# Kernel tuning notes

Measured on AMD Instinct MI355X. Metric: run time of the kernel, lower is better.

## Reference

```python
import jax, jax.numpy as jnp
import numpy as np

N = 4096          # nodes (= Mamba sequence length)
E_EDGES = 65536   # edges
D = 512           # dim_h (= d_inner, expand=1)
NEXP = 4          # num_experts (cfg.model.num_experts)
DSTATE = 16
DCONV = 4
DTRANK = 32       # ceil(D/16)
EPS = 1e-5


def _silu(x):
    return x * jax.nn.sigmoid(x)


def _bn(h, g, b):
    # BatchNorm1d over node axis (batch statistics)
    mu = h.mean(0)
    var = h.var(0)
    return (h - mu) * jax.lax.rsqrt(var + EPS) * g + b


def _mamba(u, in_w, conv_w, conv_b, x_w, dt_w, dt_b, A_log, Dp, out_w):
    # u: [L, D] single-sequence Mamba(d_model=D, d_state=16, d_conv=4, expand=1)
    L = u.shape[0]
    xz = u @ in_w                      # [L, 2D]
    xc, z = xz[:, :D], xz[:, D:]
    xp = jnp.pad(xc, ((DCONV - 1, 0), (0, 0)))
    xconv = conv_b
    for k in range(DCONV):             # depthwise causal conv, tiny fixed loop
        xconv = xconv + conv_w[:, k] * xp[k:k + L]
    xs = _silu(xconv)                  # [L, D]
    dbc = xs @ x_w                     # [L, DTRANK + 2*DSTATE]
    dt = jax.nn.softplus(dbc[:, :DTRANK] @ dt_w + dt_b)          # [L, D]
    Bm = dbc[:, DTRANK:DTRANK + DSTATE]                          # [L, S]
    Cm = dbc[:, DTRANK + DSTATE:]                                # [L, S]
    A = -jnp.exp(A_log)                                          # [D, S]
    dA = jnp.exp(dt[:, :, None] * A[None])                       # [L, D, S]
    dBu = dt[:, :, None] * Bm[:, None, :] * xs[:, :, None]       # [L, D, S]

    def step(hprev, inp):
        dA_t, dBu_t, C_t = inp
        hn = dA_t * hprev + dBu_t
        return hn, (hn * C_t[None, :]).sum(-1)

    _, ys = jax.lax.scan(step, jnp.zeros((D, DSTATE), u.dtype), (dA, dBu, Cm))
    y = ys + Dp * xs
    return (y * _silu(z)) @ out_w      # [L, D]


def setup_inputs() -> dict:
    key = jax.random.key(0)
    ks = jax.random.split(key, 24)
    s = 1.0 / np.sqrt(D)
    inp = {}
    inp['x'] = jax.random.normal(ks[0], (N, D), jnp.float32)
    inp['edge_index'] = jax.random.randint(ks[1], (2, E_EDGES), 0, N)
    inp['edge_attr'] = jax.random.normal(ks[2], (E_EDGES, D), jnp.float32)
    # GINE nn: Linear(D,D) -> ReLU -> Linear(D,D)
    inp['gin_w1'] = jax.random.normal(ks[3], (D, D)) * s
    inp['gin_b1'] = jnp.zeros((D,))
    inp['gin_w2'] = jax.random.normal(ks[4], (D, D)) * s
    inp['gin_b2'] = jnp.zeros((D,))
    # BatchNorms
    inp['bn1l_g'] = jnp.ones((D,)); inp['bn1l_b'] = jnp.zeros((D,))
    inp['bn1a_g'] = jnp.ones((D,)); inp['bn1a_b'] = jnp.zeros((D,))
    inp['bn2_g'] = jnp.ones((D,)); inp['bn2_b'] = jnp.zeros((D,))
    # gating MLP [D, D//2, NEXP]
    inp['gate_w1'] = jax.random.normal(ks[5], (D, D // 2)) * s
    inp['gate_b1'] = jnp.zeros((D // 2,))
    inp['gate_w2'] = jax.random.normal(ks[6], (D // 2, NEXP)) * (1.0 / np.sqrt(D // 2))
    inp['gate_b2'] = jnp.zeros((NEXP,))
    # stacked per-expert Mamba params
    inp['in_w'] = jax.random.normal(ks[7], (NEXP, D, 2 * D)) * s
    inp['conv_w'] = jax.random.normal(ks[8], (NEXP, D, DCONV)) * 0.5
    inp['conv_b'] = jnp.zeros((NEXP, D))
    inp['x_w'] = jax.random.normal(ks[9], (NEXP, D, DTRANK + 2 * DSTATE)) * s
    inp['dt_w'] = jax.random.normal(ks[10], (NEXP, DTRANK, D)) * (1.0 / np.sqrt(DTRANK))
    inp['dt_b'] = jax.random.normal(ks[11], (NEXP, D)) * 0.1 - 4.0
    A0 = jnp.log(jnp.arange(1, DSTATE + 1, dtype=jnp.float32))
    inp['A_log'] = jnp.broadcast_to(A0, (NEXP, D, DSTATE)).copy()
    inp['Dp'] = jnp.ones((NEXP, D))
    inp['out_w'] = jax.random.normal(ks[12], (NEXP, D, D)) * s
    # FFN
    inp['ff_w1'] = jax.random.normal(ks[13], (D, 2 * D)) * s
    inp['ff_b1'] = jnp.zeros((2 * D,))
    inp['ff_w2'] = jax.random.normal(ks[14], (2 * D, D)) * (1.0 / np.sqrt(2 * D))
    inp['ff_b2'] = jnp.zeros((D,))
    return inp


def reference(x, edge_index, edge_attr,
              gin_w1, gin_b1, gin_w2, gin_b2,
              bn1l_g, bn1l_b, bn1a_g, bn1a_b, bn2_g, bn2_b,
              gate_w1, gate_b1, gate_w2, gate_b2,
              in_w, conv_w, conv_b, x_w, dt_w, dt_b, A_log, Dp, out_w,
              ff_w1, ff_b1, ff_w2, ff_b2):
    h_in = x
    src, dst = edge_index[0], edge_index[1]
    # local GINEConv: nn(x + sum_j relu(x_j + e_ji))
    msg = jax.nn.relu(x[src] + edge_attr)                      # [E, D]
    aggr = jax.ops.segment_sum(msg, dst, num_segments=N)       # [N, D]
    h_local = jax.nn.relu((x + aggr) @ gin_w1 + gin_b1) @ gin_w2 + gin_b2
    h_local = _bn(h_in + h_local, bn1l_g, bn1l_b)
    # gated mixture of Mamba experts
    gate = jax.nn.softmax(jax.nn.relu(x @ gate_w1 + gate_b1) @ gate_w2 + gate_b2, axis=-1)  # [N, NEXP]
    ys = jax.vmap(_mamba, in_axes=(None, 0, 0, 0, 0, 0, 0, 0, 0, 0))(
        x, in_w, conv_w, conv_b, x_w, dt_w, dt_b, A_log, Dp, out_w)  # [NEXP, N, D]
    h_attn = jnp.einsum('ne,end->nd', gate, ys)
    h_attn = _bn(h_in + h_attn, bn1a_g, bn1a_b)
    # fuse + FFN
    h = h_local + h_attn
    ff = jax.nn.relu(h @ ff_w1 + ff_b1) @ ff_w2 + ff_b2
    return _bn(h + ff, bn2_g, bn2_b)
```

## Files before the change

### kernel.cpp

```cpp
#include <hip/hip_runtime.h>
#include <hip/hip_bf16.h>
#include <math.h>

#define N_NODES 4096
#define E_EDGE 65536
#define D 512
#define NEXP 4
#define DSTATE 16
#define DCONV 4
#define DTRANK 32
#define EPS 1e-5f
#define LCHUNK 32
#define NCHUNK (N_NODES / LCHUNK)

typedef __hip_bfloat16 bf16;
typedef short bf16x8 __attribute__((ext_vector_type(8)));
typedef float f32x4 __attribute__((ext_vector_type(4)));
typedef unsigned short u16x4 __attribute__((ext_vector_type(4)));

__device__ __forceinline__ float siluf(float x) { return x / (1.f + __expf(-x)); }
__device__ __forceinline__ float softplusf(float x) {
  return (x > 20.f) ? x : log1pf(__expf(x));
}
__device__ __forceinline__ unsigned short f2bf(float v) {
  bf16 b = __float2bfloat16(v);
  return *reinterpret_cast<unsigned short*>(&b);
}
__device__ __forceinline__ float bfu2f(unsigned short u) {
  bf16 b;
  *reinterpret_cast<unsigned short*>(&b) = u;
  return __bfloat162float(b);
}

__device__ __forceinline__ void gload16(const void* g, void* l) {
  __builtin_amdgcn_global_load_lds(
      (const __attribute__((address_space(1))) void*)g,
      (__attribute__((address_space(3))) void*)l, 16, 0, 0);
}

template <int FN, int EPI, bool STATS>
__global__ __launch_bounds__(256, 2) void mm_k(
    const bf16* __restrict__ A, int lda, long sA,
    const bf16* __restrict__ Bt, int ldb, long sB,
    const float* __restrict__ bias,
    float* __restrict__ Cf, bf16* __restrict__ Cb, int ldc, long sC, int K,
    const float* __restrict__ part, float* __restrict__ sacc) {
  constexpr int BN = FN * 32;
  __shared__ __align__(16) bf16 As[2][128 * 32];
  __shared__ __align__(16) bf16 Bs[2][BN * 32];
  const int z = blockIdx.z;
  A += (size_t)z * sA;
  Bt += (size_t)z * sB;
  const int tid = threadIdx.x;
  const int w = tid >> 6, l = tid & 63;
  const int wr = w >> 1, wc = w & 1;
  const int bm = blockIdx.y * 128, bn = blockIdx.x * BN;

  f32x4 acc[4][FN];
#pragma unroll
  for (int i = 0; i < 4; ++i)
#pragma unroll
    for (int j = 0; j < FN; ++j) acc[i][j] = 0.f;

  const int srow = l >> 2, schunk = l & 3;
  const bf16* gA = A + (size_t)(bm + w * 16 + srow) * lda + schunk * 8;
  const bf16* gB = Bt + (size_t)(bn + w * 16 + srow) * ldb + schunk * 8;

  const int ar = wr * 64 + (l & 15);
  const int br = wc * FN * 16 + (l & 15);
  const int kb = l >> 4;

  auto stage = [&](int b, int k0) {
    gload16(gA + k0, As[b] + w * 512);
    gload16(gA + k0 + (size_t)64 * lda, As[b] + 64 * 32 + w * 512);
    gload16(gB + k0, Bs[b] + w * 512);
    if (FN == 4) gload16(gB + k0 + (size_t)64 * ldb, Bs[b] + 64 * 32 + w * 512);
  };

  stage(0, 0);
  __syncthreads();
  int cur = 0;
  for (int k0 = 0; k0 < K; k0 += 32) {
    if (k0 + 32 < K) stage(cur ^ 1, k0 + 32);
    const bf16x8* Ap = (const bf16x8*)As[cur];
    const bf16x8* Bp = (const bf16x8*)Bs[cur];
    bf16x8 af[4], bfr[FN];
#pragma unroll
    for (int i = 0; i < 4; ++i) af[i] = Ap[(ar + i * 16) * 4 + kb];
#pragma unroll
    for (int j = 0; j < FN; ++j) bfr[j] = Bp[(br + j * 16) * 4 + kb];
#pragma unroll
    for (int i = 0; i < 4; ++i)
#pragma unroll
      for (int j = 0; j < FN; ++j)
        acc[i][j] = __builtin_amdgcn_mfma_f32_16x16x32_bf16(bfr[j], af[i], acc[i][j], 0, 0, 0);
    __syncthreads();
    cur ^= 1;
  }

  if (Cf) Cf += (size_t)z * sC;
  if (Cb) Cb += (size_t)z * sC;
  const int r0 = bm + wr * 64 + (l & 15);
  const int cb0 = bn + wc * FN * 16 + ((l >> 4) << 2);
  f32x4 ssum[FN], ssq[FN];
  if (STATS) {
#pragma unroll
    for (int j = 0; j < FN; ++j) { ssum[j] = 0.f; ssq[j] = 0.f; }
  }
#pragma unroll
  for (int i = 0; i < 4; ++i) {
    const int row = r0 + i * 16;
#pragma unroll
    for (int j = 0; j < FN; ++j) {
      const int col = cb0 + j * 16;
      f32x4 v = acc[i][j];
      if (bias) v += *(const f32x4*)&bias[col];
      if (EPI == 1) {
#pragma unroll
        for (int r = 0; r < 4; ++r) v[r] = fmaxf(v[r], 0.f);
      }
      if (Cf) *(f32x4*)&Cf[(size_t)row * ldc + col] = v;
      if (Cb) {
        u16x4 u;
#pragma unroll
        for (int r = 0; r < 4; ++r) u[r] = f2bf(v[r]);
        *(u16x4*)&Cb[(size_t)row * ldc + col] = u;
      }
      if (STATS) {
        f32x4 p = *(const f32x4*)&part[(size_t)row * ldc + col];
        f32x4 t = v + p;
        ssum[j] += t;
        ssq[j] += t * t;
      }
    }
  }
  if (STATS) {
#pragma unroll
    for (int m = 1; m < 16; m <<= 1) {
#pragma unroll
      for (int j = 0; j < FN; ++j)
#pragma unroll
        for (int r = 0; r < 4; ++r) {
          ssum[j][r] += __shfl_xor(ssum[j][r], m);
          ssq[j][r] += __shfl_xor(ssq[j][r], m);
        }
    }
    if ((l & 15) == 0) {
#pragma unroll
      for (int j = 0; j < FN; ++j)
#pragma unroll
        for (int r = 0; r < 4; ++r) {
          atomicAdd(&sacc[cb0 + j * 16 + r], ssum[j][r]);
          atomicAdd(&sacc[512 + cb0 + j * 16 + r], ssq[j][r]);
        }
    }
  }
}

struct MmArgs {
  const bf16* A[4];
  const bf16* Bt[4];
  const float* bias[4];
  float* Cf[4];
  bf16* Cb[4];
  const float* part[4];
  float* sacc[4];
  long sA[4], sB[4], sC[4];
  int lda[4], ldb[4], ldc[4], K[4], epi[4], stats[4], gx[4], cum[4];
};
__global__ __launch_bounds__(256, 2) void mgemm_k(MmArgs a) {
  __shared__ __align__(16) bf16 As[2][128 * 32];
  __shared__ __align__(16) bf16 Bs[2][64 * 32];
  int b = blockIdx.x;
  int i = 0;
  while (b >= a.cum[i]) ++i;
  int local = b - (i ? a.cum[i - 1] : 0);
  const int perz = a.gx[i] * 32;
  const int z = local / perz;
  const int rem = local - z * perz;
  const int by = rem / a.gx[i];
  const int bx = rem - by * a.gx[i];
  const int lda = a.lda[i], ldb = a.ldb[i], ldc = a.ldc[i], K = a.K[i];
  const bf16* A = a.A[i] + (size_t)z * a.sA[i];
  const bf16* Bt = a.Bt[i] + (size_t)z * a.sB[i];

  const int tid = threadIdx.x;
  const int w = tid >> 6, l = tid & 63;
  const int wr = w >> 1, wc = w & 1;
  const int bm = by * 128, bn = bx * 64;

  f32x4 acc[4][2];
#pragma unroll
  for (int p = 0; p < 4; ++p)
#pragma unroll
    for (int j = 0; j < 2; ++j) acc[p][j] = 0.f;

  const int srow = l >> 2, schunk = l & 3;
  const bf16* gA = A + (size_t)(bm + w * 16 + srow) * lda + schunk * 8;
  const bf16* gB = Bt + (size_t)(bn + w * 16 + srow) * ldb + schunk * 8;

  const int ar = wr * 64 + (l & 15);
  const int br = wc * 32 + (l & 15);
  const int kb = l >> 4;

  auto stage = [&](int bb, int k0) {
    gload16(gA + k0, As[bb] + w * 512);
    gload16(gA + k0 + (size_t)64 * lda, As[bb] + 64 * 32 + w * 512);
    gload16(gB + k0, Bs[bb] + w * 512);
  };

  stage(0, 0);
  __syncthreads();
  int cur = 0;
  for (int k0 = 0; k0 < K; k0 += 32) {
    if (k0 + 32 < K) stage(cur ^ 1, k0 + 32);
    const bf16x8* Ap = (const bf16x8*)As[cur];
    const bf16x8* Bp = (const bf16x8*)Bs[cur];
    bf16x8 af[4], bfr[2];
#pragma unroll
    for (int p = 0; p < 4; ++p) af[p] = Ap[(ar + p * 16) * 4 + kb];
#pragma unroll
    for (int j = 0; j < 2; ++j) bfr[j] = Bp[(br + j * 16) * 4 + kb];
#pragma unroll
    for (int p = 0; p < 4; ++p)
#pragma unroll
      for (int j = 0; j < 2; ++j)
        acc[p][j] = __builtin_amdgcn_mfma_f32_16x16x32_bf16(bfr[j], af[p], acc[p][j], 0, 0, 0);
    __syncthreads();
    cur ^= 1;
  }

  float* Cf = a.Cf[i] ? a.Cf[i] + (size_t)z * a.sC[i] : nullptr;
  bf16* Cb = a.Cb[i] ? a.Cb[i] + (size_t)z * a.sC[i] : nullptr;
  const float* bias = a.bias[i];
  const int epi = a.epi[i], stats = a.stats[i];
  const int r0 = bm + wr * 64 + (l & 15);
  const int cb0 = bn + wc * 32 + ((l >> 4) << 2);
  f32x4 ssum[2], ssq[2];
  ssum[0] = 0.f; ssum[1] = 0.f; ssq[0] = 0.f; ssq[1] = 0.f;
#pragma unroll
  for (int p = 0; p < 4; ++p) {
    const int row = r0 + p * 16;
#pragma unroll
    for (int j = 0; j < 2; ++j) {
      const int col = cb0 + j * 16;
      f32x4 v = acc[p][j];
      if (bias) v += *(const f32x4*)&bias[col];
      if (epi == 1) {
#pragma unroll
        for (int r = 0; r < 4; ++r) v[r] = fmaxf(v[r], 0.f);
      }
      if (Cf) *(f32x4*)&Cf[(size_t)row * ldc + col] = v;
      if (Cb) {
        u16x4 u;
#pragma unroll
        for (int r = 0; r < 4; ++r) u[r] = f2bf(v[r]);
        *(u16x4*)&Cb[(size_t)row * ldc + col] = u;
      }
      if (stats) {
        f32x4 pp = *(const f32x4*)&a.part[i][(size_t)row * ldc + col];
        f32x4 t = v + pp;
        ssum[j] += t;
        ssq[j] += t * t;
      }
    }
  }
  if (stats) {
#pragma unroll
    for (int m = 1; m < 16; m <<= 1) {
#pragma unroll
      for (int j = 0; j < 2; ++j)
#pragma unroll
        for (int r = 0; r < 4; ++r) {
          ssum[j][r] += __shfl_xor(ssum[j][r], m);
          ssq[j][r] += __shfl_xor(ssq[j][r], m);
        }
    }
    if ((l & 15) == 0) {
#pragma unroll
      for (int j = 0; j < 2; ++j)
#pragma unroll
        for (int r = 0; r < 4; ++r) {
          atomicAdd(&a.sacc[i][cb0 + j * 16 + r], ssum[j][r]);
          atomicAdd(&a.sacc[i][512 + cb0 + j * 16 + r], ssq[j][r]);
        }
    }
  }
}

struct WtArgs {
  const float* in[8];
  bf16* out[8];
  int K[8], N[8], ldo[8];
  long sin[8], sout[8];
  int cum[8];
};
__global__ __launch_bounds__(256) void wtrans_all_k(WtArgs a) {
  __shared__ float t[32][33];
  int b = blockIdx.x;
  int i = 0;
  while (b >= a.cum[i]) ++i;
  int local = b - (i ? a.cum[i - 1] : 0);
  const int ntx = a.N[i] / 32;
  const int nty = a.K[i] / 32;
  const int perz = ntx * nty;
  const int z = local / perz;
  const int rem = local - z * perz;
  const int bx = rem % ntx, by = rem / ntx;
  const float* in = a.in[i] + (size_t)z * a.sin[i];
  bf16* out = a.out[i] + (size_t)z * a.sout[i];
  const int N = a.N[i], ldo = a.ldo[i];
  const int n0 = bx * 32, k0 = by * 32;
  const int tx = threadIdx.x & 31, ty = threadIdx.x >> 5;
  for (int r = ty; r < 32; r += 8) t[r][tx] = in[(size_t)(k0 + r) * N + n0 + tx];
  __syncthreads();
  for (int r = ty; r < 32; r += 8)
    out[(size_t)(n0 + r) * ldo + k0 + tx] = __float2bfloat16(t[tx][r]);
}

__global__ void hist_k(const int* __restrict__ ei, int* __restrict__ deg) {
  int e = blockIdx.x * 256 + threadIdx.x;
  if (e < E_EDGE) atomicAdd(&deg[ei[E_EDGE + e]], 1);
}

__global__ __launch_bounds__(1024) void prefix_k(const int* __restrict__ deg,
                                                 int* __restrict__ rowstart) {
  __shared__ int s[1024];
  int t = threadIdx.x;
  int base = t * 4;
  int d0 = deg[base], d1 = deg[base + 1], d2 = deg[base + 2], d3 = deg[base + 3];
  int sum = d0 + d1 + d2 + d3;
  s[t] = sum;
  __syncthreads();
  for (int off = 1; off < 1024; off <<= 1) {
    int v = (t >= off) ? s[t - off] : 0;
    __syncthreads();
    s[t] += v;
    __syncthreads();
  }
  int excl = s[t] - sum;
  rowstart[base] = excl;
  rowstart[base + 1] = excl + d0;
  rowstart[base + 2] = excl + d0 + d1;
  rowstart[base + 3] = excl + d0 + d1 + d2;
}

__global__ void scatter_k(const int* __restrict__ ei, const int* __restrict__ rowstart,
                          int* __restrict__ cnt, int* __restrict__ eid) {
  int e = blockIdx.x * 256 + threadIdx.x;
  if (e < E_EDGE) {
    int dst = ei[E_EDGE + e];
    int slot = rowstart[dst] + atomicAdd(&cnt[dst], 1);
    eid[slot] = e;
  }
}

__global__ __launch_bounds__(256) void aggr_gather_k(
    const float* __restrict__ x, const int* __restrict__ ei, const float* __restrict__ ea,
    const int* __restrict__ rowstart, const int* __restrict__ deg,
    const int* __restrict__ eid, bf16* __restrict__ hpre, bf16* __restrict__ xbf) {
  int n = blockIdx.x;
  int tid = threadIdx.x;
  int beg = rowstart[n];
  int end = beg + deg[n];
  float a0 = 0.f, a1 = 0.f;
  int i = beg;
  for (; i + 1 < end; i += 2) {
    int e0 = eid[i], e1 = eid[i + 1];
    int s0 = ei[e0], s1 = ei[e1];
    const float* x0 = x + (size_t)s0 * D;
    const float* e0p = ea + (size_t)e0 * D;
    const float* x1 = x + (size_t)s1 * D;
    const float* e1p = ea + (size_t)e1 * D;
    a0 += fmaxf(x0[tid] + e0p[tid], 0.f) + fmaxf(x1[tid] + e1p[tid], 0.f);
    a1 += fmaxf(x0[tid + 256] + e0p[tid + 256], 0.f) +
          fmaxf(x1[tid + 256] + e1p[tid + 256], 0.f);
  }
  if (i < end) {
    int e0 = eid[i];
    int s0 = ei[e0];
    const float* x0 = x + (size_t)s0 * D;
    const float* e0p = ea + (size_t)e0 * D;
    a0 += fmaxf(x0[tid] + e0p[tid], 0.f);
    a1 += fmaxf(x0[tid + 256] + e0p[tid + 256], 0.f);
  }
  float xv0 = x[(size_t)n * D + tid];
  float xv1 = x[(size_t)n * D + tid + 256];
  hpre[(size_t)n * D + tid] = __float2bfloat16(xv0 + a0);
  hpre[(size_t)n * D + tid + 256] = __float2bfloat16(xv1 + a1);
  xbf[(size_t)n * D + tid] = __float2bfloat16(xv0);
  xbf[(size_t)n * D + tid + 256] = __float2bfloat16(xv1);
}

__global__ __launch_bounds__(256) void gate2_k(const float* __restrict__ g1,
                                               const float* __restrict__ w2,
                                               const float* __restrict__ b2,
                                               float* __restrict__ gate) {
  int row = blockIdx.x * 4 + (threadIdx.x >> 6);
  int lane = threadIdx.x & 63;
  float a0 = 0.f, a1 = 0.f, a2 = 0.f, a3 = 0.f;
  for (int k = lane; k < 256; k += 64) {
    float v = g1[(size_t)row * 256 + k];
    a0 = fmaf(v, w2[k * 4 + 0], a0);
    a1 = fmaf(v, w2[k * 4 + 1], a1);
    a2 = fmaf(v, w2[k * 4 + 2], a2);
    a3 = fmaf(v, w2[k * 4 + 3], a3);
  }
#pragma unroll
  for (int off = 32; off; off >>= 1) {
    a0 += __shfl_down(a0, off);
    a1 += __shfl_down(a1, off);
    a2 += __shfl_down(a2, off);
    a3 += __shfl_down(a3, off);
  }
  if (lane == 0) {
    float l0 = a0 + b2[0], l1 = a1 + b2[1], l2 = a2 + b2[2], l3 = a3 + b2[3];
    float m = fmaxf(fmaxf(l0, l1), fmaxf(l2, l3));
    float e0 = __expf(l0 - m), e1 = __expf(l1 - m), e2 = __expf(l2 - m), e3 = __expf(l3 - m);
    float s = 1.f / (e0 + e1 + e2 + e3);
    gate[row * 4 + 0] = e0 * s;
    gate[row * 4 + 1] = e1 * s;
    gate[row * 4 + 2] = e2 * s;
    gate[row * 4 + 3] = e3 * s;
  }
}

__global__ void conv_silu_k(const bf16* __restrict__ xz, const float* __restrict__ cw,
                            const float* __restrict__ cb, bf16* __restrict__ xs, int e0) {
  const int z = blockIdx.y;
  xz += (size_t)z * N_NODES * 2 * D;
  xs += (size_t)z * N_NODES * D;
  cw += (size_t)(e0 + z) * D * DCONV;
  cb += (size_t)(e0 + z) * D;
  int idx = blockIdx.x * blockDim.x + threadIdx.x;
  if (idx >= N_NODES * (D / 4)) return;
  int t = idx >> 7;
  int d4 = (idx & 127) << 2;
  float a[4];
#pragma unroll
  for (int j = 0; j < 4; ++j) a[j] = cb[d4 + j];
#pragma unroll
  for (int k = 0; k < DCONV; ++k) {
    int tt = t + k - (DCONV - 1);
    if (tt >= 0) {
      u16x4 v = *(const u16x4*)&xz[(size_t)tt * (2 * D) + d4];
#pragma unroll
      for (int j = 0; j < 4; ++j) a[j] = fmaf(cw[(d4 + j) * DCONV + k], bfu2f(v[j]), a[j]);
    }
  }
  u16x4 o;
#pragma unroll
  for (int j = 0; j < 4; ++j) o[j] = f2bf(siluf(a[j]));
  *(u16x4*)&xs[(size_t)t * D + d4] = o;
}

__global__ void dt_k(const float* __restrict__ dbc, const float* __restrict__ dtw,
                     const float* __restrict__ dtbias, bf16* __restrict__ dt, int e0) {
  const int z = blockIdx.y;
  dbc += (size_t)z * N_NODES * 64;
  dt += (size_t)z * N_NODES * D;
  dtw += (size_t)(e0 + z) * DTRANK * D;
  dtbias += (size_t)(e0 + z) * D;
  int idx = blockIdx.x * blockDim.x + threadIdx.x;
  if (idx >= N_NODES * (D / 4)) return;
  int t = idx >> 7;
  int d4 = (idx & 127) << 2;
  f32x4 a = *(const f32x4*)&dtbias[d4];
#pragma unroll
  for (int k = 0; k < DTRANK; ++k) {
    float b = dbc[t * 64 + k];
    f32x4 wv = *(const f32x4*)&dtw[k * D + d4];
    a += b * wv;
  }
  u16x4 o;
#pragma unroll
  for (int j = 0; j < 4; ++j) o[j] = f2bf(softplusf(a[j]));
  *(u16x4*)&dt[(size_t)t * D + d4] = o;
}

__device__ __forceinline__ void bn_params(const float* acc, int d, float& mu, float& rsig) {
  mu = acc[d] * (1.f / N_NODES);
  float var = acc[512 + d] * (1.f / N_NODES) - mu * mu;
  rsig = rsqrtf(var + EPS);
}

__global__ void norm_k(const float* __restrict__ p, const float* __restrict__ q,
                       const float* __restrict__ acc, const float* __restrict__ g,
                       const float* __restrict__ b, float* __restrict__ o) {
  int idx = blockIdx.x * blockDim.x + threadIdx.x;
  if (idx >= N_NODES * D) return;
  int d = idx & (D - 1);
  float mu, rsig;
  bn_params(acc, d, mu, rsig);
  o[idx] = (p[idx] + q[idx] - mu) * rsig * g[d] + b[d];
}

__global__ void bnadd2_k(const float* __restrict__ x, const float* __restrict__ hloc,
                         const float* __restrict__ hattn, const float* __restrict__ acc1,
                         const float* __restrict__ acc2, const float* __restrict__ g1,
                         const float* __restrict__ b1, const float* __restrict__ g2,
                         const float* __restrict__ b2, float* __restrict__ of,
                         bf16* __restrict__ ob) {
  int idx = blockIdx.x * blockDim.x + threadIdx.x;
  if (idx >= N_NODES * D) return;
  int d = idx & (D - 1);
  float mu1, rs1, mu2, rs2;
  bn_params(acc1, d, mu1, rs1);
  bn_params(acc2, d, mu2, rs2);
  float xv = x[idx];
  float v = (xv + hloc[idx] - mu1) * rs1 * g1[d] + b1[d] +
            (xv + hattn[idx] - mu2) * rs2 * g2[d] + b2[d];
  of[idx] = v;
  ob[idx] = __float2bfloat16(v);
}

__global__ __launch_bounds__(512) void scanA_k(const bf16* __restrict__ dt,
                                               const bf16* __restrict__ xs,
                                               const float* __restrict__ dbc,
                                               const float* __restrict__ Alog,
                                               float* __restrict__ Q,
                                               float* __restrict__ dtsum, int e0) {
  const int z = blockIdx.y;
  dt += (size_t)z * N_NODES * D;
  xs += (size_t)z * N_NODES * D;
  dbc += (size_t)z * N_NODES * 64;
  Alog += (size_t)(e0 + z) * D * DSTATE;
  Q += (size_t)z * NCHUNK * D * DSTATE;
  dtsum += (size_t)z * NCHUNK * D;
  int c = blockIdx.x;
  int d = threadIdx.x;
  float As[DSTATE], h[DSTATE];
#pragma unroll
  for (int s = 0; s < DSTATE; ++s) {
    As[s] = -__expf(Alog[d * DSTATE + s]);
    h[s] = 0.f;
  }
  float dts = 0.f;
  int t0 = c * LCHUNK;
  for (int t = t0; t < t0 + LCHUNK; ++t) {
    float dtv = __bfloat162float(dt[(size_t)t * D + d]);
    float xv = __bfloat162float(xs[(size_t)t * D + d]);
    float bx = dtv * xv;
    dts += dtv;
#pragma unroll
    for (int s = 0; s < DSTATE; ++s) {
      float Bv = dbc[(size_t)t * 64 + DTRANK + s];
      h[s] = fmaf(__expf(dtv * As[s]), h[s], bx * Bv);
    }
  }
  size_t base = ((size_t)c * D + d) * DSTATE;
#pragma unroll
  for (int s = 0; s < DSTATE; ++s) Q[base + s] = h[s];
  dtsum[c * D + d] = dts;
}

__global__ __launch_bounds__(256) void scanB_k(const float* __restrict__ Q,
                                               const float* __restrict__ dtsum,
                                               const float* __restrict__ Alog,
                                               float* __restrict__ Hin, int e0) {
  const int z = blockIdx.y;
  Q += (size_t)z * NCHUNK * D * DSTATE;
  dtsum += (size_t)z * NCHUNK * D;
  Alog += (size_t)(e0 + z) * D * DSTATE;
  Hin += (size_t)z * NCHUNK * D * DSTATE;
  int idx = blockIdx.x * blockDim.x + threadIdx.x;
  int d = idx >> 4;
  float As = -__expf(Alog[idx]);
  float h = 0.f;
  for (int c = 0; c < NCHUNK; ++c) {
    size_t base = (size_t)c * D * DSTATE + idx;
    Hin[base] = h;
    h = fmaf(__expf(As * dtsum[c * D + d]), h, Q[base]);
  }
}

__global__ __launch_bounds__(512) void scanC_k(const bf16* __restrict__ dt,
                                               const bf16* __restrict__ xs,
                                               const float* __restrict__ dbc,
                                               const float* __restrict__ Alog,
                                               const float* __restrict__ Hin,
                                               const bf16* __restrict__ xz,
                                               const float* __restrict__ Dp,
                                               const float* __restrict__ gate,
                                               bf16* __restrict__ u, int e0) {
  const int z = blockIdx.y;
  dt += (size_t)z * N_NODES * D;
  xs += (size_t)z * N_NODES * D;
  dbc += (size_t)z * N_NODES * 64;
  Alog += (size_t)(e0 + z) * D * DSTATE;
  Hin += (size_t)z * NCHUNK * D * DSTATE;
  xz += (size_t)z * N_NODES * 2 * D;
  Dp += (size_t)(e0 + z) * D;
  u += (size_t)(e0 + z) * 512;
  const int ge = e0 + z;
  int c = blockIdx.x;
  int d = threadIdx.x;
  float As[DSTATE], h[DSTATE];
  size_t base = ((size_t)c * D + d) * DSTATE;
#pragma unroll
  for (int s = 0; s < DSTATE; ++s) {
    As[s] = -__expf(Alog[d * DSTATE + s]);
    h[s] = Hin[base + s];
  }
  float Dv = Dp[d];
  int t0 = c * LCHUNK;
  for (int t = t0; t < t0 + LCHUNK; ++t) {
    float dtv = __bfloat162float(dt[(size_t)t * D + d]);
    float xv = __bfloat162float(xs[(size_t)t * D + d]);
    float bx = dtv * xv;
    float y = 0.f;
#pragma unroll
    for (int s = 0; s < DSTATE; ++s) {
      float Bv = dbc[(size_t)t * 64 + DTRANK + s];
      float Cv = dbc[(size_t)t * 64 + DTRANK + DSTATE + s];
      h[s] = fmaf(__expf(dtv * As[s]), h[s], bx * Bv);
      y = fmaf(h[s], Cv, y);
    }
    float zv = __bfloat162float(xz[(size_t)t * (2 * D) + D + d]);
    float gv = gate[t * NEXP + ge];
    u[(size_t)t * 2048 + d] = __float2bfloat16(gv * (y + Dv * xv) * siluf(zv));
  }
}

extern "C" void kernel_launch(void* const* d_in, const int* in_sizes, int n_in,
                              void* d_out, int out_size, void* d_ws, size_t ws_size,
                              hipStream_t stream) {
  const float* x = (const float*)d_in[0];
  const int* ei = (const int*)d_in[1];
  const float* ea = (const float*)d_in[2];
  const float* gin_w1 = (const float*)d_in[3];
  const float* gin_b1 = (const float*)d_in[4];
  const float* gin_w2 = (const float*)d_in[5];
  const float* gin_b2 = (const float*)d_in[6];
  const float* bn1l_g = (const float*)d_in[7];
  const float* bn1l_b = (const float*)d_in[8];
  const float* bn1a_g = (const float*)d_in[9];
  const float* bn1a_b = (const float*)d_in[10];
  const float* bn2_g = (const float*)d_in[11];
  const float* bn2_b = (const float*)d_in[12];
  const float* gate_w1 = (const float*)d_in[13];
  const float* gate_b1 = (const float*)d_in[14];
  const float* gate_w2 = (const float*)d_in[15];
  const float* gate_b2 = (const float*)d_in[16];
  const float* in_w = (const float*)d_in[17];
  const float* conv_w = (const float*)d_in[18];
  const float* conv_b = (const float*)d_in[19];
  const float* x_w = (const float*)d_in[20];
  const float* dt_w = (const float*)d_in[21];
  const float* dt_b = (const float*)d_in[22];
  const float* A_log = (const float*)d_in[23];
  const float* Dp = (const float*)d_in[24];
  const float* out_w = (const float*)d_in[25];
  const float* ff_w1 = (const float*)d_in[26];
  const float* ff_b1 = (const float*)d_in[27];
  const float* ff_w2 = (const float*)d_in[28];
  const float* ff_b2 = (const float*)d_in[29];
  float* out = (float*)d_out;

  const size_t ND = (size_t)N_NODES * D;
  const size_t NDb = ND / 2;

  const size_t fixed_f = 3 * ND + (size_t)N_NODES * 256 + 16384 + 2490624 + ND + 2048 +
                         81920 + 2 * ND + 4096;
  const size_t per_f = 2 * ND + NDb + (size_t)N_NODES * 64 + NDb +
                       2 * (size_t)NCHUNK * D * DSTATE + (size_t)NCHUNK * D;
  const int EB = (ws_size >= (fixed_f + 4 * per_f + 65536) * sizeof(float)) ? 4 : 1;

  float* ws = (float*)d_ws;
  size_t off = 0;
  auto alloc = [&](size_t n) {
    float* p = ws + off;
    off += (n + 63) & ~(size_t)63;
    return p;
  };
  float* ffo = alloc(ND);
  float* pbuf = alloc(ND);
  float* hlocal = alloc(ND);
  float* g1 = alloc((size_t)N_NODES * 256);
  float* gate = alloc((size_t)N_NODES * NEXP);
  bf16* gw1t = (bf16*)alloc(131072);
  bf16* gw2t = (bf16*)alloc(131072);
  bf16* gatew1t = (bf16*)alloc(65536);
  bf16* inwt = (bf16*)alloc(1048576);
  bf16* xwt = (bf16*)alloc(65536);
  bf16* outwt_cat = (bf16*)alloc(524288);
  bf16* ffw1t = (bf16*)alloc(262144);
  bf16* ffw2t = (bf16*)alloc(262144);
  int* deg = (int*)alloc(N_NODES);
  int* cnt = (int*)alloc(N_NODES);
  float* accs = alloc(3072);
  int* eid = (int*)alloc(E_EDGE);
  int* rowstart = (int*)alloc(N_NODES);
  float* xbf_f = alloc(NDb);
  float* xz_f = alloc((size_t)EB * ND);
  float* xs_f = alloc((size_t)EB * NDb);
  float* dbc = alloc((size_t)EB * N_NODES * 64);
  float* dtb_f = alloc((size_t)EB * NDb);
  float* Qb = alloc((size_t)EB * NCHUNK * D * DSTATE);
  float* Hin = alloc((size_t)EB * NCHUNK * D * DSTATE);
  float* dtsum = alloc((size_t)EB * NCHUNK * D);
  float* ucat_f = alloc(4 * NDb);
  float* hattn_raw = alloc(ND);
  float* acc1 = accs, *acc2 = accs + 1024, *acc3 = accs + 2048;

  bf16* x_bf = (bf16*)xbf_f;
  bf16* hpre_bf = (bf16*)pbuf;
  bf16* t1_bf = (bf16*)(pbuf + NDb);
  bf16* xz_bf = (bf16*)xz_f;
  bf16* xs_bf = (bf16*)xs_f;
  bf16* dt_bf = (bf16*)dtb_f;
  bf16* ucat = (bf16*)ucat_f;
  float* hcomb = xz_f;
  bf16* hcomb_bf = (bf16*)(ucat_f);
  bf16* ffh_bf = (bf16*)pbuf;

  const int nelem = N_NODES * D;
  const int ew = (nelem + 255) / 256;
  const int ew4 = (nelem / 4 + 255) / 256;

  hipMemsetAsync(deg, 0, (N_NODES + N_NODES + 3072) * sizeof(float), stream);

  WtArgs wa;
  const float* wsrc[8] = {gin_w1, gin_w2, gate_w1, in_w, x_w, out_w, ff_w1, ff_w2};
  bf16* wdst[8] = {gw1t, gw2t, gatew1t, inwt, xwt, outwt_cat, ffw1t, ffw2t};
  int wK[8] = {512, 512, 512, 512, 512, 512, 512, 1024};
  int wN[8] = {512, 512, 256, 1024, 64, 512, 1024, 512};
  int wldo[8] = {512, 512, 512, 512, 512, 2048, 512, 1024};
  long wsin[8] = {0, 0, 0, (long)512 * 1024, (long)512 * 64, (long)512 * 512, 0, 0};
  long wsout[8] = {0, 0, 0, (long)512 * 1024, (long)64 * 512, 512, 0, 0};
  int wz[8] = {1, 1, 1, 4, 4, 4, 1, 1};
  int cum = 0;
  for (int i = 0; i < 8; ++i) {
    wa.in[i] = wsrc[i];
    wa.out[i] = wdst[i];
    wa.K[i] = wK[i];
    wa.N[i] = wN[i];
    wa.ldo[i] = wldo[i];
    wa.sin[i] = wsin[i];
    wa.sout[i] = wsout[i];
    cum += (wN[i] / 32) * (wK[i] / 32) * wz[i];
    wa.cum[i] = cum;
  }
  wtrans_all_k<<<cum, 256, 0, stream>>>(wa);

  hist_k<<<E_EDGE / 256, 256, 0, stream>>>(ei, deg);
  prefix_k<<<1, 1024, 0, stream>>>(deg, rowstart);
  scatter_k<<<E_EDGE / 256, 256, 0, stream>>>(ei, rowstart, cnt, eid);
  aggr_gather_k<<<N_NODES, 256, 0, stream>>>(x, ei, ea, rowstart, deg, eid, hpre_bf, x_bf);

  if (EB == 4) {
    MmArgs m1 = {};
    m1.A[0] = hpre_bf; m1.lda[0] = 512; m1.sA[0] = 0;
    m1.Bt[0] = gw1t; m1.ldb[0] = 512; m1.sB[0] = 0;
    m1.bias[0] = gin_b1; m1.Cb[0] = t1_bf; m1.ldc[0] = 512; m1.sC[0] = 0;
    m1.K[0] = 512; m1.epi[0] = 1; m1.gx[0] = 8;
    m1.A[1] = x_bf; m1.lda[1] = 512; m1.sA[1] = 0;
    m1.Bt[1] = gatew1t; m1.ldb[1] = 512; m1.sB[1] = 0;
    m1.bias[1] = gate_b1; m1.Cf[1] = g1; m1.ldc[1] = 256; m1.sC[1] = 0;
    m1.K[1] = 512; m1.epi[1] = 1; m1.gx[1] = 4;
    m1.A[2] = x_bf; m1.lda[2] = 512; m1.sA[2] = 0;
    m1.Bt[2] = inwt; m1.ldb[2] = 512; m1.sB[2] = (long)512 * 1024;
    m1.Cb[2] = xz_bf; m1.ldc[2] = 1024; m1.sC[2] = (long)N_NODES * 1024;
    m1.K[2] = 512; m1.epi[2] = 0; m1.gx[2] = 16;
    int c1 = 8 * 32;
    m1.cum[0] = c1;
    c1 += 4 * 32;
    m1.cum[1] = c1;
    c1 += 16 * 32 * 4;
    m1.cum[2] = c1;
    m1.cum[3] = c1;
    mgemm_k<<<c1, 256, 0, stream>>>(m1);
    gate2_k<<<N_NODES / 4, 256, 0, stream>>>(g1, gate_w2, gate_b2, gate);
    conv_silu_k<<<dim3(ew4, 4), 256, 0, stream>>>(xz_bf, conv_w, conv_b, xs_bf, 0);

    MmArgs m2 = {};
    m2.A[0] = t1_bf; m2.lda[0] = 512; m2.sA[0] = 0;
    m2.Bt[0] = gw2t; m2.ldb[0] = 512; m2.sB[0] = 0;
    m2.bias[0] = gin_b2; m2.Cf[0] = hlocal; m2.ldc[0] = 512; m2.sC[0] = 0;
    m2.K[0] = 512; m2.epi[0] = 0; m2.stats[0] = 1; m2.part[0] = x; m2.sacc[0] = acc1;
    m2.gx[0] = 8;
    m2.A[1] = xs_bf; m2.lda[1] = 512; m2.sA[1] = (long)ND;
    m2.Bt[1] = xwt; m2.ldb[1] = 512; m2.sB[1] = (long)64 * 512;
    m2.Cf[1] = dbc; m2.ldc[1] = 64; m2.sC[1] = (long)N_NODES * 64;
    m2.K[1] = 512; m2.epi[1] = 0; m2.gx[1] = 1;
    int c2 = 8 * 32;
    m2.cum[0] = c2;
    c2 += 1 * 32 * 4;
    m2.cum[1] = c2;
    m2.cum[2] = c2;
    m2.cum[3] = c2;
    mgemm_k<<<c2, 256, 0, stream>>>(m2);

    dt_k<<<dim3(ew4, 4), 256, 0, stream>>>(dbc, dt_w, dt_b, dt_bf, 0);
    scanA_k<<<dim3(NCHUNK, 4), 512, 0, stream>>>(dt_bf, xs_bf, dbc, A_log, Qb, dtsum, 0);
    scanB_k<<<dim3((D * DSTATE) / 256, 4), 256, 0, stream>>>(Qb, dtsum, A_log, Hin, 0);
    scanC_k<<<dim3(NCHUNK, 4), 512, 0, stream>>>(dt_bf, xs_bf, dbc, A_log, Hin, xz_bf, Dp,
                                                 gate, ucat, 0);
  } else {
    mm_k<2, 1, false><<<dim3(8, 32, 1), 256, 0, stream>>>(
        hpre_bf, 512, 0, gw1t, 512, 0, gin_b1, nullptr, t1_bf, 512, 0, 512, nullptr,
        nullptr);
    mm_k<2, 0, true><<<dim3(8, 32, 1), 256, 0, stream>>>(
        t1_bf, 512, 0, gw2t, 512, 0, gin_b2, hlocal, nullptr, 512, 0, 512, x, acc1);
    mm_k<2, 1, false><<<dim3(4, 32, 1), 256, 0, stream>>>(
        x_bf, 512, 0, gatew1t, 512, 0, gate_b1, g1, nullptr, 256, 0, 512, nullptr,
        nullptr);
    gate2_k<<<N_NODES / 4, 256, 0, stream>>>(g1, gate_w2, gate_b2, gate);
    for (int e0 = 0; e0 < NEXP; ++e0) {
      mm_k<4, 0, false><<<dim3(8, 32, 1), 256, 0, stream>>>(
          x_bf, 512, 0, inwt + (size_t)e0 * 512 * 1024, 512, 0, nullptr, nullptr, xz_bf,
          1024, 0, 512, nullptr, nullptr);
      conv_silu_k<<<dim3(ew4, 1), 256, 0, stream>>>(xz_bf, conv_w, conv_b, xs_bf, e0);
      mm_k<2, 0, false><<<dim3(1, 32, 1), 256, 0, stream>>>(
          xs_bf, 512, 0, xwt + (size_t)e0 * 64 * 512, 512, 0, nullptr, dbc, nullptr, 64,
          0, 512, nullptr, nullptr);
      dt_k<<<dim3(ew4, 1), 256, 0, stream>>>(dbc, dt_w, dt_b, dt_bf, e0);
      scanA_k<<<dim3(NCHUNK, 1), 512, 0, stream>>>(dt_bf, xs_bf, dbc, A_log, Qb, dtsum, e0);
      scanB_k<<<dim3((D * DSTATE) / 256, 1), 256, 0, stream>>>(Qb, dtsum, A_log, Hin, e0);
      scanC_k<<<dim3(NCHUNK, 1), 512, 0, stream>>>(dt_bf, xs_bf, dbc, A_log, Hin, xz_bf,
                                                   Dp, gate, ucat, e0);
    }
  }

  mm_k<2, 0, true><<<dim3(8, 32, 1), 256, 0, stream>>>(
      ucat, 2048, 0, outwt_cat, 2048, 0, nullptr, hattn_raw, nullptr, 512, 0, 2048, x,
      acc2);

  bnadd2_k<<<ew, 256, 0, stream>>>(x, hlocal, hattn_raw, acc1, acc2, bn1l_g, bn1l_b,
                                   bn1a_g, bn1a_b, hcomb, hcomb_bf);
  mm_k<4, 1, false><<<dim3(8, 32, 1), 256, 0, stream>>>(
      hcomb_bf, 512, 0, ffw1t, 512, 0, ff_b1, nullptr, ffh_bf, 1024, 0, 512, nullptr,
      nullptr);
  mm_k<2, 0, true><<<dim3(8, 32, 1), 256, 0, stream>>>(
      ffh_bf, 1024, 0, ffw2t, 1024, 0, ff_b2, ffo, nullptr, 512, 0, 1024, hcomb, acc3);
  norm_k<<<ew, 256, 0, stream>>>(hcomb, ffo, acc3, bn2_g, bn2_b, out);
}
```

Baseline: 457.9 us.

## Vectorize edge gather and BN kernels, fuse gate softmax into conv launch

The edge aggregation kernel now splits each node's edges across two 128-thread halves. Each thread does float4 loads of x and edge_attr, and the two halves combine through shared memory. The batch-norm elementwise kernels (norm and bnadd2) now process four elements per thread with vector loads and stores. The gate softmax kernel is folded into the conv+SiLU launch as an extra grid row, which removes one launch. The aim is wider memory transactions and fewer launches. The cost is that half of each block idles in the aggregation epilogue, and the merged grid has many early-exit blocks.

```diff
diff --git a/kernel.cpp b/kernel.cpp
--- a/kernel.cpp
+++ b/kernel.cpp
@@ -359,44 +359,43 @@
     const float* __restrict__ x, const int* __restrict__ ei, const float* __restrict__ ea,
     const int* __restrict__ rowstart, const int* __restrict__ deg,
     const int* __restrict__ eid, bf16* __restrict__ hpre, bf16* __restrict__ xbf) {
-  int n = blockIdx.x;
-  int tid = threadIdx.x;
-  int beg = rowstart[n];
-  int end = beg + deg[n];
-  float a0 = 0.f, a1 = 0.f;
-  int i = beg;
-  for (; i + 1 < end; i += 2) {
-    int e0 = eid[i], e1 = eid[i + 1];
-    int s0 = ei[e0], s1 = ei[e1];
-    const float* x0 = x + (size_t)s0 * D;
-    const float* e0p = ea + (size_t)e0 * D;
-    const float* x1 = x + (size_t)s1 * D;
-    const float* e1p = ea + (size_t)e1 * D;
-    a0 += fmaxf(x0[tid] + e0p[tid], 0.f) + fmaxf(x1[tid] + e1p[tid], 0.f);
-    a1 += fmaxf(x0[tid + 256] + e0p[tid + 256], 0.f) +
-          fmaxf(x1[tid + 256] + e1p[tid + 256], 0.f);
-  }
-  if (i < end) {
-    int e0 = eid[i];
-    int s0 = ei[e0];
-    const float* x0 = x + (size_t)s0 * D;
-    const float* e0p = ea + (size_t)e0 * D;
-    a0 += fmaxf(x0[tid] + e0p[tid], 0.f);
-    a1 += fmaxf(x0[tid + 256] + e0p[tid + 256], 0.f);
-  }
-  float xv0 = x[(size_t)n * D + tid];
-  float xv1 = x[(size_t)n * D + tid + 256];
-  hpre[(size_t)n * D + tid] = __float2bfloat16(xv0 + a0);
-  hpre[(size_t)n * D + tid + 256] = __float2bfloat16(xv1 + a1);
-  xbf[(size_t)n * D + tid] = __float2bfloat16(xv0);
-  xbf[(size_t)n * D + tid + 256] = __float2bfloat16(xv1);
-}
-
-__global__ __launch_bounds__(256) void gate2_k(const float* __restrict__ g1,
-                                               const float* __restrict__ w2,
-                                               const float* __restrict__ b2,
-                                               float* __restrict__ gate) {
-  int row = blockIdx.x * 4 + (threadIdx.x >> 6);
+  __shared__ float comb[512];
+  const int n = blockIdx.x;
+  const int sub = threadIdx.x >> 7;
+  const int lane = threadIdx.x & 127;
+  const int d4 = lane << 2;
+  const int beg = rowstart[n];
+  const int end = beg + deg[n];
+  f32x4 a = 0.f;
+  for (int i = beg + sub; i < end; i += 2) {
+    const int e = eid[i];
+    const int s = ei[e];
+    f32x4 xv = *(const f32x4*)&x[(size_t)s * D + d4];
+    f32x4 ev = *(const f32x4*)&ea[(size_t)e * D + d4];
+#pragma unroll
+    for (int j = 0; j < 4; ++j) a[j] += fmaxf(xv[j] + ev[j], 0.f);
+  }
+  if (sub == 0) *(f32x4*)&comb[d4] = a;
+  __syncthreads();
+  if (sub == 1) {
+    a += *(const f32x4*)&comb[d4];
+    f32x4 xn = *(const f32x4*)&x[(size_t)n * D + d4];
+    u16x4 h, xb;
+#pragma unroll
+    for (int j = 0; j < 4; ++j) {
+      h[j] = f2bf(xn[j] + a[j]);
+      xb[j] = f2bf(xn[j]);
+    }
+    *(u16x4*)&hpre[(size_t)n * D + d4] = h;
+    *(u16x4*)&xbf[(size_t)n * D + d4] = xb;
+  }
+}
+
+__device__ __forceinline__ void gate2_body(const float* __restrict__ g1,
+                                           const float* __restrict__ w2,
+                                           const float* __restrict__ b2,
+                                           float* __restrict__ gate, int blk) {
+  int row = blk * 4 + (threadIdx.x >> 6);
   int lane = threadIdx.x & 63;
   float a0 = 0.f, a1 = 0.f, a2 = 0.f, a3 = 0.f;
   for (int k = lane; k < 256; k += 64) {
@@ -425,14 +424,22 @@
   }
 }
 
-__global__ void conv_silu_k(const bf16* __restrict__ xz, const float* __restrict__ cw,
-                            const float* __restrict__ cb, bf16* __restrict__ xs, int e0) {
-  const int z = blockIdx.y;
+__global__ __launch_bounds__(256) void gate2_k(const float* __restrict__ g1,
+                                               const float* __restrict__ w2,
+                                               const float* __restrict__ b2,
+                                               float* __restrict__ gate) {
+  gate2_body(g1, w2, b2, gate, blockIdx.x);
+}
+
+__device__ __forceinline__ void conv_body(const bf16* __restrict__ xz,
+                                          const float* __restrict__ cw,
+                                          const float* __restrict__ cb,
+                                          bf16* __restrict__ xs, int z, int e0, int bx) {
   xz += (size_t)z * N_NODES * 2 * D;
   xs += (size_t)z * N_NODES * D;
   cw += (size_t)(e0 + z) * D * DCONV;
   cb += (size_t)(e0 + z) * D;
-  int idx = blockIdx.x * blockDim.x + threadIdx.x;
+  int idx = bx * 256 + threadIdx.x;
   if (idx >= N_NODES * (D / 4)) return;
   int t = idx >> 7;
   int d4 = (idx & 127) << 2;
@@ -452,6 +459,23 @@
 #pragma unroll
   for (int j = 0; j < 4; ++j) o[j] = f2bf(siluf(a[j]));
   *(u16x4*)&xs[(size_t)t * D + d4] = o;
+}
+
+__global__ void conv_silu_k(const bf16* __restrict__ xz, const float* __restrict__ cw,
+                            const float* __restrict__ cb, bf16* __restrict__ xs, int e0) {
+  conv_body(xz, cw, cb, xs, blockIdx.y, e0, blockIdx.x);
+}
+
+__global__ __launch_bounds__(256) void convgate_k(
+    const bf16* __restrict__ xz, const float* __restrict__ cw,
+    const float* __restrict__ cb, bf16* __restrict__ xs,
+    const float* __restrict__ g1, const float* __restrict__ w2,
+    const float* __restrict__ b2, float* __restrict__ gate) {
+  if (blockIdx.y == 4) {
+    if (blockIdx.x < N_NODES / 4) gate2_body(g1, w2, b2, gate, blockIdx.x);
+    return;
+  }
+  conv_body(xz, cw, cb, xs, blockIdx.y, 0, blockIdx.x);
 }
 
 __global__ void dt_k(const float* __restrict__ dbc, const float* __restrict__ dtw,
@@ -488,11 +512,21 @@
                        const float* __restrict__ acc, const float* __restrict__ g,
                        const float* __restrict__ b, float* __restrict__ o) {
   int idx = blockIdx.x * blockDim.x + threadIdx.x;
-  if (idx >= N_NODES * D) return;
-  int d = idx & (D - 1);
-  float mu, rsig;
-  bn_params(acc, d, mu, rsig);
-  o[idx] = (p[idx] + q[idx] - mu) * rsig * g[d] + b[d];
+  if (idx >= N_NODES * (D / 4)) return;
+  int d4 = (idx & 127) << 2;
+  size_t base = (size_t)idx << 2;
+  f32x4 pv = *(const f32x4*)&p[base];
+  f32x4 qv = *(const f32x4*)&q[base];
+  f32x4 gv = *(const f32x4*)&g[d4];
+  f32x4 bv = *(const f32x4*)&b[d4];
+  f32x4 ov;
+#pragma unroll
+  for (int j = 0; j < 4; ++j) {
+    float mu, rs;
+    bn_params(acc, d4 + j, mu, rs);
+    ov[j] = (pv[j] + qv[j] - mu) * rs * gv[j] + bv[j];
+  }
+  *(f32x4*)&o[base] = ov;
 }
 
 __global__ void bnadd2_k(const float* __restrict__ x, const float* __restrict__ hloc,
@@ -502,16 +536,30 @@
                          const float* __restrict__ b2, float* __restrict__ of,
                          bf16* __restrict__ ob) {
   int idx = blockIdx.x * blockDim.x + threadIdx.x;
-  if (idx >= N_NODES * D) return;
-  int d = idx & (D - 1);
-  float mu1, rs1, mu2, rs2;
-  bn_params(acc1, d, mu1, rs1);
-  bn_params(acc2, d, mu2, rs2);
-  float xv = x[idx];
-  float v = (xv + hloc[idx] - mu1) * rs1 * g1[d] + b1[d] +
-            (xv + hattn[idx] - mu2) * rs2 * g2[d] + b2[d];
-  of[idx] = v;
-  ob[idx] = __float2bfloat16(v);
+  if (idx >= N_NODES * (D / 4)) return;
+  int d4 = (idx & 127) << 2;
+  size_t base = (size_t)idx << 2;
+  f32x4 xv = *(const f32x4*)&x[base];
+  f32x4 hl = *(const f32x4*)&hloc[base];
+  f32x4 ha = *(const f32x4*)&hattn[base];
+  f32x4 g1v = *(const f32x4*)&g1[d4];
+  f32x4 b1v = *(const f32x4*)&b1[d4];
+  f32x4 g2v = *(const f32x4*)&g2[d4];
+  f32x4 b2v = *(const f32x4*)&b2[d4];
+  f32x4 ov;
+  u16x4 obv;
+#pragma unroll
+  for (int j = 0; j < 4; ++j) {
+    float mu1, rs1, mu2, rs2;
+    bn_params(acc1, d4 + j, mu1, rs1);
+    bn_params(acc2, d4 + j, mu2, rs2);
+    float v = (xv[j] + hl[j] - mu1) * rs1 * g1v[j] + b1v[j] +
+              (xv[j] + ha[j] - mu2) * rs2 * g2v[j] + b2v[j];
+    ov[j] = v;
+    obv[j] = f2bf(v);
+  }
+  *(f32x4*)&of[base] = ov;
+  *(u16x4*)&ob[base] = obv;
 }
 
 __global__ __launch_bounds__(512) void scanA_k(const bf16* __restrict__ dt,
@@ -715,7 +763,6 @@
   bf16* ffh_bf = (bf16*)pbuf;
 
   const int nelem = N_NODES * D;
-  const int ew = (nelem + 255) / 256;
   const int ew4 = (nelem / 4 + 255) / 256;
 
   hipMemsetAsync(deg, 0, (N_NODES + N_NODES + 3072) * sizeof(float), stream);
@@ -770,8 +817,8 @@
     m1.cum[2] = c1;
     m1.cum[3] = c1;
     mgemm_k<<<c1, 256, 0, stream>>>(m1);
-    gate2_k<<<N_NODES / 4, 256, 0, stream>>>(g1, gate_w2, gate_b2, gate);
-    conv_silu_k<<<dim3(ew4, 4), 256, 0, stream>>>(xz_bf, conv_w, conv_b, xs_bf, 0);
+    convgate_k<<<dim3(ew4, 5), 256, 0, stream>>>(xz_bf, conv_w, conv_b, xs_bf, g1,
+                                                 gate_w2, gate_b2, gate);
 
     MmArgs m2 = {};
     m2.A[0] = t1_bf; m2.lda[0] = 512; m2.sA[0] = 0;
@@ -826,12 +873,12 @@
       ucat, 2048, 0, outwt_cat, 2048, 0, nullptr, hattn_raw, nullptr, 512, 0, 2048, x,
       acc2);
 
-  bnadd2_k<<<ew, 256, 0, stream>>>(x, hlocal, hattn_raw, acc1, acc2, bn1l_g, bn1l_b,
-                                   bn1a_g, bn1a_b, hcomb, hcomb_bf);
+  bnadd2_k<<<ew4, 256, 0, stream>>>(x, hlocal, hattn_raw, acc1, acc2, bn1l_g, bn1l_b,
+                                    bn1a_g, bn1a_b, hcomb, hcomb_bf);
   mm_k<4, 1, false><<<dim3(8, 32, 1), 256, 0, stream>>>(
       hcomb_bf, 512, 0, ffw1t, 512, 0, ff_b1, nullptr, ffh_bf, 1024, 0, 512, nullptr,
       nullptr);
   mm_k<2, 0, true><<<dim3(8, 32, 1), 256, 0, stream>>>(
       ffh_bf, 1024, 0, ffw2t, 1024, 0, ff_b2, ffo, nullptr, 512, 0, 1024, hcomb, acc3);
-  norm_k<<<ew, 256, 0, stream>>>(hcomb, ffo, acc3, bn2_g, bn2_b, out);
-}
+  norm_k<<<ew4, 256, 0, stream>>>(hcomb, ffo, acc3, bn2_g, bn2_b, out);
+}
```

Result: no change. 459.7 us (+0.4%).
